# Optimization experiments

Hardware: AMD Instinct MI355X
Metric: run time of the kernel (lower is better)

The kernel has to match this reference:

```python
import jax, jax.numpy as jnp
import numpy as np
from itertools import product

D = 96  # input grid resolution; after subdivision it is 2*D = 192
N_VOX = 20000
C_IN = 64
C_OUT = 64

OFFSETS = jnp.array(list(product([-1, 0, 1], repeat=3)), dtype=jnp.int32)   # [27,3] conv neighborhood
CHILD = jnp.array(list(product([0, 1], repeat=3)), dtype=jnp.int32)        # [8,3] subdivision children


def _lin(coords, d):
    # linearize (z,y,x)-style coords into a flat index for the dense lookup grid
    return (coords[:, 0] * d + coords[:, 1]) * d + coords[:, 2]


def _submanifold_conv3d(coords, feats, W, b, d):
    """Submanifold sparse 3x3x3 conv: output only at active sites.
    coords: [N,3] int32, feats: [N,Cin], W: [27,Cin,Cout], b: [Cout]."""
    n = coords.shape[0]
    grid = jnp.full((d * d * d,), -1, dtype=jnp.int32).at[_lin(coords, d)].set(
        jnp.arange(n, dtype=jnp.int32))
    out = jnp.broadcast_to(b, (n, b.shape[0])).astype(feats.dtype)
    for k in range(27):  # fixed small kernel loop (unrolled under jit)
        nb = coords + OFFSETS[k]
        inb = jnp.all((nb >= 0) & (nb < d), axis=1)
        idx = grid[_lin(jnp.clip(nb, 0, d - 1), d)]
        mask = (inb & (idx >= 0)).astype(feats.dtype)
        f = feats[jnp.maximum(idx, 0)] * mask[:, None]  # gather active neighbors
        out = out + f @ W[k]
    return out


def setup_inputs() -> dict:
    rng = np.random.default_rng(0)
    lin = rng.choice(D ** 3, size=N_VOX, replace=False)  # unique active voxels
    coords = np.stack([lin // (D * D), (lin // D) % D, lin % D], axis=1).astype(np.int32)
    key = jax.random.key(0)
    k1, k2, k3, k4, k5 = jax.random.split(key, 5)
    scale = 1.0 / np.sqrt(27.0 * C_IN)
    return {
        "coords": jnp.asarray(coords),
        "feats": jax.random.normal(k1, (N_VOX, C_IN), jnp.float32),
        "W1": jax.random.normal(k2, (27, C_IN, C_OUT), jnp.float32) * scale,
        "b1": jax.random.normal(k3, (C_OUT,), jnp.float32) * 0.01,
        "W2": jax.random.normal(k4, (27, C_OUT, C_OUT), jnp.float32) * scale,
        "b2": jax.random.normal(k5, (C_OUT,), jnp.float32) * 0.01,
    }


def reference(coords, feats, W1, b1, W2, b2):
    # act_layers: SparseConv3d + SiLU
    h = jax.nn.silu(_submanifold_conv3d(coords, feats, W1, b1, D))
    n = coords.shape[0]
    coords2 = ((coords * 2)[:, None, :] + CHILD[None, :, :]).reshape(8 * n, 3)
    h2 = jnp.repeat(h, 8, axis=0)  # matches (N,8,C)->(8N,C) child order
    # out_layers: SparseConv3d + SiLU at doubled resolution
    return jax.nn.silu(_submanifold_conv3d(coords2, h2, W2, b2, 2 * D))
```

## Files before the change

kernel.cpp:

```cpp
#include <hip/hip_runtime.h>

#define D1 96
#define GRID_VOX (D1 * D1 * D1)
#define CAP2S 8
#define OS 68

typedef __attribute__((ext_vector_type(8))) short short8_t;
typedef __attribute__((ext_vector_type(4))) float f32x4;

__device__ __forceinline__ unsigned short bf16rne(float x) {
    unsigned u = __float_as_uint(x);
    return (unsigned short)((u + 0x7FFF + ((u >> 16) & 1)) >> 16);
}
__device__ __forceinline__ void split2(float v, unsigned short& hi,
                                       unsigned short& lo) {
    hi = bf16rne(v);
    float hf = __uint_as_float((unsigned)hi << 16);
    lo = bf16rne(v - hf);
}
__device__ __forceinline__ float silu(float v) {
    return v / (1.f + __expf(-v));
}

__global__ void setup_kernel(const float* __restrict__ W1,
                             const float* __restrict__ W2,
                             const int* __restrict__ coords,
                             unsigned short* __restrict__ grid,
                             unsigned short* __restrict__ Wpk1h,
                             unsigned short* __restrict__ Wpk1l,
                             unsigned short* __restrict__ Wpk2h,
                             unsigned short* __restrict__ Wpk2l,
                             float* __restrict__ W2e, int n) {
    int t = blockIdx.x * blockDim.x + threadIdx.x;
    if (t < 512) {
        int fid = t >> 6, l = t & 63;
        int kb = fid >> 2, c = fid & 3;
#pragma unroll
        for (int e = 0; e < 8; ++e) {
            int ci = kb * 32 + ((l >> 4) << 3) + e;
            int co = c * 16 + (l & 15);
            unsigned short hi, lo;
            split2(W1[13 * 4096 + ci * 64 + co], hi, lo);
            Wpk1h[(size_t)t * 8 + e] = hi;
            Wpk1l[(size_t)t * 8 + e] = lo;
        }
    } else if (t < 4608) {
        int u = t - 512;
        int fid = u >> 6, l = u & 63;
        int s = fid >> 3, kb = (fid >> 2) & 1, c = fid & 3;
        int s0 = (s >> 2) & 1, s1 = (s >> 1) & 1, s2 = s & 1;
#pragma unroll
        for (int e = 0; e < 8; ++e) {
            int ci = kb * 32 + ((l >> 4) << 3) + e;
            int co = c * 16 + (l & 15);
            float sum = 0.f;
            for (int o0 = -s0; o0 <= 1 - s0; ++o0)
                for (int o1 = -s1; o1 <= 1 - s1; ++o1)
                    for (int o2 = -s2; o2 <= 1 - s2; ++o2) {
                        int k = (o0 + 1) * 9 + (o1 + 1) * 3 + (o2 + 1);
                        sum += W2[k * 4096 + ci * 64 + co];
                    }
            unsigned short hi, lo;
            split2(sum, hi, lo);
            Wpk2h[(size_t)u * 8 + e] = hi;
            Wpk2l[(size_t)u * 8 + e] = lo;
        }
    } else if (t < 4608 + 262144) {
        int r = t - 4608;
        int sd = r >> 12, e = r & 4095;
        int s = sd >> 3, d = sd & 7;
        int sa[3] = { (s >> 2) & 1, (s >> 1) & 1, s & 1 };
        int da[3] = { (d >> 2) & 1, (d >> 1) & 1, d & 1 };
        int lo_[3], hi_[3];
        for (int a = 0; a < 3; ++a) {
            int p = sa[a] - 1 + da[a];
            int l = 2 * p - sa[a];     if (l < -1) l = -1;
            int h = 2 * p + 1 - sa[a]; if (h > 1) h = 1;
            lo_[a] = l; hi_[a] = h;
        }
        float sum = 0.f;
        for (int o0 = lo_[0]; o0 <= hi_[0]; ++o0)
            for (int o1 = lo_[1]; o1 <= hi_[1]; ++o1)
                for (int o2 = lo_[2]; o2 <= hi_[2]; ++o2) {
                    int k = (o0 + 1) * 9 + (o1 + 1) * 3 + (o2 + 1);
                    sum += W2[k * 4096 + e];
                }
        W2e[(size_t)sd * 4096 + e] = sum;
    } else {
        int i = t - (4608 + 262144);
        if (i < n)
            grid[(coords[3 * i] * D1 + coords[3 * i + 1]) * D1 +
                 coords[3 * i + 2]] = (unsigned short)(i + 1);
    }
}

__device__ __forceinline__ void load_split_A(const float* __restrict__ src,
                                             int arow, int lane, short8_t& ah0,
                                             short8_t& al0, short8_t& ah1,
                                             short8_t& al1) {
    const float* ap = src + (size_t)arow * 64 + ((lane >> 4) << 3);
    f32x4 a0 = *(const f32x4*)(ap);
    f32x4 a1 = *(const f32x4*)(ap + 4);
    f32x4 a2 = *(const f32x4*)(ap + 32);
    f32x4 a3 = *(const f32x4*)(ap + 36);
#pragma unroll
    for (int e = 0; e < 4; ++e) {
        unsigned short hh, ll;
        split2(a0[e], hh, ll); ah0[e] = (short)hh; al0[e] = (short)ll;
        split2(a1[e], hh, ll); ah0[4 + e] = (short)hh; al0[4 + e] = (short)ll;
        split2(a2[e], hh, ll); ah1[e] = (short)hh; al1[e] = (short)ll;
        split2(a3[e], hh, ll); ah1[4 + e] = (short)hh; al1[4 + e] = (short)ll;
    }
}

__device__ __forceinline__ void dense_mfma8(const short8_t ah0, const short8_t al0,
                                            const short8_t ah1, const short8_t al1,
                                            const short8_t* __restrict__ Bh,
                                            const short8_t* __restrict__ Bl,
                                            const float* __restrict__ bias,
                                            float* __restrict__ oT, int w,
                                            int lane) {
    int c0 = (w >> 2) * 2;
#pragma unroll
    for (int cc = 0; cc < 2; ++cc) {
        int c = c0 + cc;
        short8_t bh0 = Bh[c * 64 + lane];
        short8_t bl0 = Bl[c * 64 + lane];
        short8_t bh1 = Bh[(4 + c) * 64 + lane];
        short8_t bl1 = Bl[(4 + c) * 64 + lane];
        f32x4 acc = {0.f, 0.f, 0.f, 0.f};
        acc = __builtin_amdgcn_mfma_f32_16x16x32_bf16(ah0, bh0, acc, 0, 0, 0);
        acc = __builtin_amdgcn_mfma_f32_16x16x32_bf16(al0, bh0, acc, 0, 0, 0);
        acc = __builtin_amdgcn_mfma_f32_16x16x32_bf16(ah0, bl0, acc, 0, 0, 0);
        acc = __builtin_amdgcn_mfma_f32_16x16x32_bf16(ah1, bh1, acc, 0, 0, 0);
        acc = __builtin_amdgcn_mfma_f32_16x16x32_bf16(al1, bh1, acc, 0, 0, 0);
        acc = __builtin_amdgcn_mfma_f32_16x16x32_bf16(ah1, bl1, acc, 0, 0, 0);
        int col = c * 16 + (lane & 15);
        float bb = bias[col];
#pragma unroll
        for (int r = 0; r < 4; ++r) {
            int row = (w & 3) * 16 + ((lane >> 4) << 2) + r;
            oT[row * OS + col] = acc[r] + bb;
        }
    }
}

__device__ __forceinline__ void scan64(int cnt, int lane, int* pfxs, int* cnts,
                                       int* nps) {
    int val = cnt;
#pragma unroll
    for (int off = 1; off < 64; off <<= 1) {
        int v2 = __shfl_up(val, off);
        if (lane >= off) val += v2;
    }
    pfxs[lane] = val - cnt;
    cnts[lane] = cnt;
    if (lane == 63) nps[0] = val;
}

__device__ __forceinline__ void fixup_loop(const float* __restrict__ src,
                                           const float* __restrict__ Wbase,
                                           const int* __restrict__ pl, int np,
                                           float fsc[8][2][64],
                                           float* __restrict__ oT, int w,
                                           int lane) {
    int it = 0;
#pragma unroll 1
    for (int p = w; p < np; p += 8, ++it) {
        int e = pl[p];
        int j = e & 0x1FFFF, tag = (e >> 17) & 31, row = (e >> 23) & 63;
        float fv = src[(size_t)j * 64 + lane];
        int buf = it & 1;
        fsc[w][buf][lane] = fv;
        const float* wk = Wbase + (size_t)tag * 4096;
        float a0 = 0.f, a1 = 0.f, a2 = 0.f, a3 = 0.f;
#pragma unroll
        for (int c4 = 0; c4 < 16; ++c4) {
            f32x4 fb = *(f32x4*)&fsc[w][buf][c4 * 4];
            a0 += fb[0] * wk[(c4 * 4 + 0) * 64 + lane];
            a1 += fb[1] * wk[(c4 * 4 + 1) * 64 + lane];
            a2 += fb[2] * wk[(c4 * 4 + 2) * 64 + lane];
            a3 += fb[3] * wk[(c4 * 4 + 3) * 64 + lane];
        }
        atomicAdd(&oT[row * OS + lane], (a0 + a1) + (a2 + a3));
    }
}

__global__ __launch_bounds__(512) void conv1_fused_kernel(
    const int* __restrict__ coords, const float* __restrict__ feats,
    const float* __restrict__ W1, const unsigned short* __restrict__ Wpk1h,
    const unsigned short* __restrict__ Wpk1l, const float* __restrict__ b1,
    const unsigned short* __restrict__ grid, int* __restrict__ c2s,
    int* __restrict__ p2s, float* __restrict__ h, int n) {
    __shared__ __align__(16) float oT[64 * OS];
    __shared__ __align__(16) float fsc[8][2][64];
    __shared__ int plt[64 * 26];
    __shared__ int pl[1664];
    __shared__ int pfxs[64], cnts_s[64], nps[1];
    int base = blockIdx.x * 64;
    int t = threadIdx.x, w = t >> 6, lane = t & 63;

    if (t < 64) {
        int myv = base + t;
        int cnt = 0;
        if (myv < n) {
            int c0 = coords[3 * myv], c1v = coords[3 * myv + 1],
                c2v = coords[3 * myv + 2];
            int n2[8] = {0, 0, 0, 0, 0, 0, 0, 0};
#pragma unroll 1
            for (int g = 0; g < 3; ++g) {
                int jv9[9];
                int kb = g * 9;
#pragma unroll
                for (int u = 0; u < 9; ++u) {
                    int k = kb + u;
                    int o0 = k / 9 - 1, o1 = (k / 3) % 3 - 1, o2 = k % 3 - 1;
                    int x0 = c0 + o0, x1 = c1v + o1, x2 = c2v + o2;
                    bool inb = (unsigned)x0 < D1 && (unsigned)x1 < D1 &&
                               (unsigned)x2 < D1;
                    jv9[u] = inb ? (int)grid[(x0 * D1 + x1) * D1 + x2] : 0;
                }
#pragma unroll
                for (int u = 0; u < 9; ++u) {
                    int k = kb + u;
                    if (k == 13) continue;
                    int j1 = jv9[u];
                    if (j1 < 1 || j1 > n) continue;
                    int o0 = k / 9 - 1, o1 = (k / 3) % 3 - 1, o2 = k % 3 - 1;
                    int x0 = c0 + o0, x1 = c1v + o1, x2 = c2v + o2;
                    int jj = j1 - 1;
                    if (coords[3 * jj] != x0 || coords[3 * jj + 1] != x1 ||
                        coords[3 * jj + 2] != x2)
                        continue;
                    plt[t * 26 + cnt] = jj | (k << 17);
                    ++cnt;
#pragma unroll
                    for (int s = 0; s < 8; ++s) {
                        int d0 = o0 + 1 - ((s >> 2) & 1);
                        int d1 = o1 + 1 - ((s >> 1) & 1);
                        int d2 = o2 + 1 - (s & 1);
                        if (((d0 | d1 | d2) & ~1) == 0) {
                            int d = (d0 << 2) | (d1 << 1) | d2;
                            p2s[((size_t)myv * 8 + s) * CAP2S + n2[s]] =
                                jj | (d << 17);
                            ++n2[s];
                        }
                    }
                }
            }
#pragma unroll
            for (int s = 0; s < 8; ++s) c2s[myv * 8 + s] = n2[s];
        }
        scan64(cnt, lane, pfxs, cnts_s, nps);
    }

    int arow = base + (w & 3) * 16 + (lane & 15);
    if (arow >= n) arow = n - 1;
    short8_t ah0, al0, ah1, al1;
    load_split_A(feats, arow, lane, ah0, al0, ah1, al1);
    dense_mfma8(ah0, al0, ah1, al1, (const short8_t*)Wpk1h,
                (const short8_t*)Wpk1l, b1, oT, w, lane);
    __syncthreads();

    {
        int row = t & 63, e0 = t >> 6;
        int cr = cnts_s[row], pf = pfxs[row];
        for (int e = e0; e < cr; e += 8)
            pl[pf + e] = plt[row * 26 + e] | (row << 23);
    }
    __syncthreads();

    fixup_loop(feats, W1, pl, nps[0], fsc, oT, w, lane);
    __syncthreads();

    {
        int r = t >> 3, c8 = (t & 7) * 8;
        if (base + r < n) {
#pragma unroll
            for (int jj = 0; jj < 2; ++jj) {
                f32x4 v = *(f32x4*)&oT[r * OS + c8 + jj * 4];
#pragma unroll
                for (int u = 0; u < 4; ++u) v[u] = silu(v[u]);
                *(f32x4*)&h[(size_t)(base + r) * 64 + c8 + jj * 4] = v;
            }
        }
    }
}

__global__ __launch_bounds__(512) void conv2_fused_kernel(
    const float* __restrict__ h, const unsigned short* __restrict__ Wpk2h,
    const unsigned short* __restrict__ Wpk2l, const float* __restrict__ W2e,
    const float* __restrict__ b2, const int* __restrict__ c2s,
    const int* __restrict__ p2s, float* __restrict__ out, int n) {
    __shared__ __align__(16) float oT[64 * OS];
    __shared__ __align__(16) float fsc[8][2][64];
    __shared__ int pl[448];
    __shared__ int pfxs[64], cnts_s[64], nps[1];
    int base = blockIdx.x * 64, s = blockIdx.y;
    int t = threadIdx.x, w = t >> 6, lane = t & 63;

    if (t < 64) {
        int cnt = (base + lane < n) ? c2s[(size_t)(base + lane) * 8 + s] : 0;
        scan64(cnt, lane, pfxs, cnts_s, nps);
    }

    int arow = base + (w & 3) * 16 + (lane & 15);
    if (arow >= n) arow = n - 1;
    short8_t ah0, al0, ah1, al1;
    load_split_A(h, arow, lane, ah0, al0, ah1, al1);
    dense_mfma8(ah0, al0, ah1, al1,
                (const short8_t*)Wpk2h + (size_t)s * 8 * 64,
                (const short8_t*)Wpk2l + (size_t)s * 8 * 64, b2, oT, w, lane);
    __syncthreads();

    {
        int row = t & 63, e0 = t >> 6;
        int cr = cnts_s[row], pf = pfxs[row];
        for (int e = e0; e < cr; e += 8)
            pl[pf + e] =
                p2s[((size_t)(base + row) * 8 + s) * CAP2S + e] | (row << 23);
    }
    __syncthreads();

    fixup_loop(h, W2e + (size_t)s * 8 * 4096, pl, nps[0], fsc, oT, w, lane);
    __syncthreads();

    {
        int r = t >> 3, c8 = (t & 7) * 8;
        if (base + r < n) {
#pragma unroll
            for (int jj = 0; jj < 2; ++jj) {
                f32x4 v = *(f32x4*)&oT[r * OS + c8 + jj * 4];
#pragma unroll
                for (int u = 0; u < 4; ++u) v[u] = silu(v[u]);
                *(f32x4*)&out[((size_t)(base + r) * 8 + s) * 64 + c8 + jj * 4] = v;
            }
        }
    }
}

extern "C" void kernel_launch(void* const* d_in, const int* in_sizes, int n_in,
                              void* d_out, int out_size, void* d_ws,
                              size_t ws_size, hipStream_t stream) {
    const int* coords = (const int*)d_in[0];
    const float* feats = (const float*)d_in[1];
    const float* W1 = (const float*)d_in[2];
    const float* b1 = (const float*)d_in[3];
    const float* W2 = (const float*)d_in[4];
    const float* b2 = (const float*)d_in[5];
    float* out = (float*)d_out;

    int n = in_sizes[0] / 3;
    int nblk = (n + 63) / 64;

    char* ws = (char*)d_ws;
    size_t off = 0;
    auto alloc = [&](size_t bytes) {
        size_t o = off;
        off = (off + bytes + 255) & ~(size_t)255;
        return o;
    };
    unsigned short* grid1 = (unsigned short*)(ws + alloc((size_t)GRID_VOX * 2));
    float* h      = (float*)(ws + alloc((size_t)n * 64 * 4));
    float* W2e    = (float*)(ws + alloc(64 * 4096 * 4));
    unsigned short* Wpk1h = (unsigned short*)(ws + alloc(512 * 8 * 2));
    unsigned short* Wpk1l = (unsigned short*)(ws + alloc(512 * 8 * 2));
    unsigned short* Wpk2h = (unsigned short*)(ws + alloc(4096 * 8 * 2));
    unsigned short* Wpk2l = (unsigned short*)(ws + alloc(4096 * 8 * 2));
    int*   c2s    = (int*)(ws + alloc((size_t)n * 8 * 4));
    int*   p2s    = (int*)(ws + alloc((size_t)n * 8 * CAP2S * 4));

    int totalT = 4608 + 262144 + n;
    setup_kernel<<<(totalT + 255) / 256, 256, 0, stream>>>(
        W1, W2, coords, grid1, Wpk1h, Wpk1l, Wpk2h, Wpk2l, W2e, n);

    conv1_fused_kernel<<<nblk, 512, 0, stream>>>(coords, feats, W1, Wpk1h,
                                                 Wpk1l, b1, grid1, c2s, p2s, h,
                                                 n);
    conv2_fused_kernel<<<dim3(nblk, 8), 512, 0, stream>>>(
        h, Wpk2h, Wpk2l, W2e, b2, c2s, p2s, out, n);
}
```

Measured before the change: 83.42 us.

## Process two child subdivisions per conv2 block with split wave groups

The conv2 kernel now handles two child slots per block, with each group of four waves doing the dense MFMA, fixup and output for one child. The grid's y dimension halves and the h row tile is shared across both children. The intent is fewer blocks, amortised setup and better reuse of the A tile. The cost is twice the shared memory (oT and pl are doubled), fewer waves per child for the fixup loop, and a dense MFMA loop that is no longer unrolled.

```diff
diff --git a/kernel.cpp b/kernel.cpp
--- a/kernel.cpp
+++ b/kernel.cpp
@@ -110,6 +110,36 @@
         split2(a1[e], hh, ll); ah0[4 + e] = (short)hh; al0[4 + e] = (short)ll;
         split2(a2[e], hh, ll); ah1[e] = (short)hh; al1[e] = (short)ll;
         split2(a3[e], hh, ll); ah1[4 + e] = (short)hh; al1[4 + e] = (short)ll;
+    }
+}
+
+__device__ __forceinline__ void dense_mfma4(const short8_t ah0, const short8_t al0,
+                                            const short8_t ah1, const short8_t al1,
+                                            const short8_t* __restrict__ Bh,
+                                            const short8_t* __restrict__ Bl,
+                                            const float* __restrict__ bias,
+                                            float* __restrict__ oT, int wl,
+                                            int lane) {
+#pragma unroll 1
+    for (int c = 0; c < 4; ++c) {
+        short8_t bh0 = Bh[c * 64 + lane];
+        short8_t bl0 = Bl[c * 64 + lane];
+        short8_t bh1 = Bh[(4 + c) * 64 + lane];
+        short8_t bl1 = Bl[(4 + c) * 64 + lane];
+        f32x4 acc = {0.f, 0.f, 0.f, 0.f};
+        acc = __builtin_amdgcn_mfma_f32_16x16x32_bf16(ah0, bh0, acc, 0, 0, 0);
+        acc = __builtin_amdgcn_mfma_f32_16x16x32_bf16(al0, bh0, acc, 0, 0, 0);
+        acc = __builtin_amdgcn_mfma_f32_16x16x32_bf16(ah0, bl0, acc, 0, 0, 0);
+        acc = __builtin_amdgcn_mfma_f32_16x16x32_bf16(ah1, bh1, acc, 0, 0, 0);
+        acc = __builtin_amdgcn_mfma_f32_16x16x32_bf16(al1, bh1, acc, 0, 0, 0);
+        acc = __builtin_amdgcn_mfma_f32_16x16x32_bf16(ah1, bl1, acc, 0, 0, 0);
+        int col = c * 16 + (lane & 15);
+        float bb = bias[col];
+#pragma unroll
+        for (int r = 0; r < 4; ++r) {
+            int row = wl * 16 + ((lane >> 4) << 2) + r;
+            oT[row * OS + col] = acc[r] + bb;
+        }
     }
 }
 
@@ -161,22 +191,22 @@
 __device__ __forceinline__ void fixup_loop(const float* __restrict__ src,
                                            const float* __restrict__ Wbase,
                                            const int* __restrict__ pl, int np,
-                                           float fsc[8][2][64],
-                                           float* __restrict__ oT, int w,
-                                           int lane) {
+                                           float* __restrict__ myfsc,
+                                           float* __restrict__ oT, int w0,
+                                           int stride, int lane) {
     int it = 0;
 #pragma unroll 1
-    for (int p = w; p < np; p += 8, ++it) {
+    for (int p = w0; p < np; p += stride, ++it) {
         int e = pl[p];
         int j = e & 0x1FFFF, tag = (e >> 17) & 31, row = (e >> 23) & 63;
         float fv = src[(size_t)j * 64 + lane];
         int buf = it & 1;
-        fsc[w][buf][lane] = fv;
+        myfsc[buf * 64 + lane] = fv;
         const float* wk = Wbase + (size_t)tag * 4096;
         float a0 = 0.f, a1 = 0.f, a2 = 0.f, a3 = 0.f;
 #pragma unroll
         for (int c4 = 0; c4 < 16; ++c4) {
-            f32x4 fb = *(f32x4*)&fsc[w][buf][c4 * 4];
+            f32x4 fb = *(f32x4*)&myfsc[buf * 64 + c4 * 4];
             a0 += fb[0] * wk[(c4 * 4 + 0) * 64 + lane];
             a1 += fb[1] * wk[(c4 * 4 + 1) * 64 + lane];
             a2 += fb[2] * wk[(c4 * 4 + 2) * 64 + lane];
@@ -270,7 +300,7 @@
     }
     __syncthreads();
 
-    fixup_loop(feats, W1, pl, nps[0], fsc, oT, w, lane);
+    fixup_loop(feats, W1, pl, nps[0], &fsc[w][0][0], oT, w, 8, lane);
     __syncthreads();
 
     {
@@ -292,48 +322,56 @@
     const unsigned short* __restrict__ Wpk2l, const float* __restrict__ W2e,
     const float* __restrict__ b2, const int* __restrict__ c2s,
     const int* __restrict__ p2s, float* __restrict__ out, int n) {
-    __shared__ __align__(16) float oT[64 * OS];
+    __shared__ __align__(16) float oT[2][64 * OS];
     __shared__ __align__(16) float fsc[8][2][64];
-    __shared__ int pl[448];
-    __shared__ int pfxs[64], cnts_s[64], nps[1];
-    int base = blockIdx.x * 64, s = blockIdx.y;
+    __shared__ int pl[2][448];
+    __shared__ int pfxs[2][64], cnts_s[2][64], nps[2];
+    int base = blockIdx.x * 64;
+    int s0 = blockIdx.y * 2;
     int t = threadIdx.x, w = t >> 6, lane = t & 63;
-
-    if (t < 64) {
+    int sg = w >> 2, wl = w & 3;
+    int s = s0 + sg;
+
+    if (wl == 0) {
         int cnt = (base + lane < n) ? c2s[(size_t)(base + lane) * 8 + s] : 0;
-        scan64(cnt, lane, pfxs, cnts_s, nps);
-    }
-
-    int arow = base + (w & 3) * 16 + (lane & 15);
+        scan64(cnt, lane, pfxs[sg], cnts_s[sg], &nps[sg]);
+    }
+
+    int arow = base + wl * 16 + (lane & 15);
     if (arow >= n) arow = n - 1;
     short8_t ah0, al0, ah1, al1;
     load_split_A(h, arow, lane, ah0, al0, ah1, al1);
-    dense_mfma8(ah0, al0, ah1, al1,
+    dense_mfma4(ah0, al0, ah1, al1,
                 (const short8_t*)Wpk2h + (size_t)s * 8 * 64,
-                (const short8_t*)Wpk2l + (size_t)s * 8 * 64, b2, oT, w, lane);
+                (const short8_t*)Wpk2l + (size_t)s * 8 * 64, b2, oT[sg], wl,
+                lane);
     __syncthreads();
 
     {
-        int row = t & 63, e0 = t >> 6;
-        int cr = cnts_s[row], pf = pfxs[row];
-        for (int e = e0; e < cr; e += 8)
-            pl[pf + e] =
-                p2s[((size_t)(base + row) * 8 + s) * CAP2S + e] | (row << 23);
-    }
-    __syncthreads();
-
-    fixup_loop(h, W2e + (size_t)s * 8 * 4096, pl, nps[0], fsc, oT, w, lane);
+        int child = t >> 8, row = (t >> 2) & 63, e0 = t & 3;
+        int cr = cnts_s[child][row], pf = pfxs[child][row];
+        int sc = s0 + child;
+        for (int e = e0; e < cr; e += 4)
+            pl[child][pf + e] =
+                p2s[((size_t)(base + row) * 8 + sc) * CAP2S + e] | (row << 23);
+    }
+    __syncthreads();
+
+    fixup_loop(h, W2e + (size_t)s * 8 * 4096, pl[sg], nps[sg], &fsc[w][0][0],
+               oT[sg], wl, 4, lane);
     __syncthreads();
 
     {
-        int r = t >> 3, c8 = (t & 7) * 8;
+        int child = t >> 8, tid = t & 255;
+        int r = tid >> 2, c16 = (tid & 3) * 16;
         if (base + r < n) {
-#pragma unroll
-            for (int jj = 0; jj < 2; ++jj) {
-                f32x4 v = *(f32x4*)&oT[r * OS + c8 + jj * 4];
+            size_t orow = ((size_t)(base + r) * 8 + s0 + child) * 64;
+#pragma unroll
+            for (int jj = 0; jj < 4; ++jj) {
+                f32x4 v = *(f32x4*)&oT[child][r * OS + c16 + jj * 4];
 #pragma unroll
                 for (int u = 0; u < 4; ++u) v[u] = silu(v[u]);
-                *(f32x4*)&out[((size_t)(base + r) * 8 + s) * 64 + c8 + jj * 4] = v;
+                *(f32x4*)&out[orow + c16 + jj * 4] = v;
             }
         }
     }
@@ -377,6 +415,6 @@
     conv1_fused_kernel<<<nblk, 512, 0, stream>>>(coords, feats, W1, Wpk1h,
                                                  Wpk1l, b1, grid1, c2s, p2s, h,
                                                  n);
-    conv2_fused_kernel<<<dim3(nblk, 8), 512, 0, stream>>>(
+    conv2_fused_kernel<<<dim3(nblk, 4), 512, 0, stream>>>(
         h, Wpk2h, Wpk2l, W2e, b2, c2s, p2s, out, n);
 }
```

Measured after the change: 89.20 us. +6.9%, slower.
